# Optimization experiments

Hardware: AMD Instinct MI355X
Metric: run time of the kernel (lower is better)

The kernel has to match this reference:

```python
import jax, jax.numpy as jnp
import numpy as np
from jax import lax

# Module dims (match init_kwargs / input_specs)
CIN, COUT, K, STRIDE = 8, 16, 3, 2
U = V = 32                      # input spatial size (inshape = (CIN, U, V))
UO = VO = U // STRIDE           # 'same' padding with stride -> 16
IN_DIM = CIN * U * V + 1        # 8193 (homogeneous)
OUT_DIM = COUT * UO * VO + 1    # 4097 (homogeneous)
N = 1024                        # batch (columns of x_affine)


def setup_inputs() -> dict:
    key = jax.random.key(0)
    k1, k2, k3, k4, k5 = jax.random.split(key, 5)
    w = jax.random.normal(k1, (COUT, CIN, K, K), dtype=jnp.float32) * 0.1
    b = jax.random.normal(k2, (COUT,), dtype=jnp.float32) * 0.1
    # Keying matrices (dense stand-ins for the sparse keys); scaled to keep values sane.
    A = jax.random.normal(k3, (OUT_DIM, OUT_DIM), dtype=jnp.float32) / np.sqrt(OUT_DIM)
    Ainv = jax.random.normal(k4, (IN_DIM, IN_DIM), dtype=jnp.float32) / np.sqrt(IN_DIM)
    x_affine = jax.random.normal(k5, (IN_DIM, N), dtype=jnp.float32)
    return {"w": w, "b": b, "A": A, "Ainv": Ainv, "x_affine": x_affine}


def _toeplitz_conv_apply(z, w, b):
    """Apply the affine Toeplitz conv matrix T to z of shape (CIN*U*V+1, N).
    T = [[conv, bias], [0, 1]] so T@z = [conv(z[:-1]) + b*z[-1]; z[-1]]."""
    n = z.shape[1]
    hom = z[-1]                                   # (N,) homogeneous row
    x = z[:-1].T.reshape(n, CIN, U, V)            # (N, CIN, U, V)
    y = lax.conv_general_dilated(
        x, w, window_strides=(STRIDE, STRIDE), padding="SAME",
        dimension_numbers=("NCHW", "OIHW", "NCHW"))  # (N, COUT, UO, VO)
    y = y + b[None, :, None, None] * hom[:, None, None, None]
    yf = y.reshape(n, COUT * UO * VO).T           # (COUT*UO*VO, N)
    return jnp.concatenate([yf, hom[None, :]], axis=0)  # (OUT_DIM, N)


def reference(w, b, A, Ainv, x_affine):
    # What @ x = A @ T @ Ainv @ x  (factored; never materializes What)
    z = Ainv @ x_affine                # (IN_DIM, N)
    t = _toeplitz_conv_apply(z, w, b)  # (OUT_DIM, N)
    return A @ t                       # (OUT_DIM, N)
```

## Files before the change

### kernel.cpp

```cpp
#include <hip/hip_runtime.h>

#define IN_DIM 8193
#define OUT_DIM 4097
#define NB 1024
#define M1 8192
#define KP1 8256
#define M2 4096
#define KP2 4160

typedef __attribute__((ext_vector_type(8))) short short8;
typedef __attribute__((ext_vector_type(4))) float f32x4;

__device__ __forceinline__ unsigned short f2bf(float f) {
  unsigned int u = __float_as_uint(f);
  u = (u + 0x7fffu + ((u >> 16) & 1u)) >> 16;
  return (unsigned short)u;
}
__device__ __forceinline__ float bf2f(unsigned short u) {
  return __uint_as_float(((unsigned int)u) << 16);
}

__global__ __launch_bounds__(256) void cvt_pad_kernel(
    const float* __restrict__ src, unsigned short* __restrict__ dst,
    int sR, int sC, int dR, int dC) {
  int gid = blockIdx.x * 256 + threadIdx.x;
  int i4 = gid * 4;
  if (i4 >= dR * dC) return;
  int r = i4 / dC;
  int c = i4 - r * dC;
  unsigned short o[4];
#pragma unroll
  for (int j = 0; j < 4; ++j) {
    int cc = c + j;
    float v = (r < sR && cc < sC) ? src[(size_t)r * sC + cc] : 0.f;
    o[j] = f2bf(v);
  }
  unsigned int lo = (unsigned)o[0] | ((unsigned)o[1] << 16);
  unsigned int hi = (unsigned)o[2] | ((unsigned)o[3] << 16);
  *reinterpret_cast<uint2*>(dst + i4) = make_uint2(lo, hi);
}

__global__ __launch_bounds__(256) void transpose_cvt_zh_kernel(
    const float* __restrict__ src, unsigned short* __restrict__ dst,
    const float* __restrict__ arow, float* __restrict__ zh,
    int K, int N, int Kp) {
  __shared__ float tl[32][33];
  const int ntk = Kp >> 5;
  int bx = blockIdx.x % ntk;
  int by = blockIdx.x / ntk;
  int k0 = bx * 32, n0 = by * 32;
  int tx = threadIdx.x & 31, ty = threadIdx.x >> 5;
#pragma unroll
  for (int i = 0; i < 4; ++i) {
    int k = k0 + ty + i * 8;
    tl[ty + i * 8][tx] = (k < K) ? src[(size_t)k * N + n0 + tx] : 0.f;
  }
  const float av = (k0 + tx < K) ? arow[k0 + tx] : 0.f;
  __syncthreads();
#pragma unroll
  for (int i = 0; i < 4; ++i) {
    int n = n0 + ty + i * 8;
    float v = tl[tx][ty + i * 8];
    dst[(size_t)n * Kp + k0 + tx] = f2bf(v);
    float c = av * v;
#pragma unroll
    for (int m = 1; m <= 16; m <<= 1) c += __shfl_xor(c, m);
    if (tx == 0) atomicAdd(&zh[n], c);
  }
}

__global__ __launch_bounds__(256) void zero_kernel(float4* __restrict__ p, int n) {
  int i = blockIdx.x * 256 + threadIdx.x;
  if (i < n) p[i] = make_float4(0.f, 0.f, 0.f, 0.f);
}

template <int NKT, int NSPLIT, int BMBITS, int MROWS>
__global__ __launch_bounds__(512) void gemm_dp(
    const unsigned short* __restrict__ Ab,
    const unsigned short* __restrict__ Bt,
    float* __restrict__ C, int Kp) {
  extern __shared__ unsigned short lds[];
  const int tid = threadIdx.x;
  const int wid = tid >> 6;
  const int lane = tid & 63;
  const int b = blockIdx.x;
  const int x = b & 7, q = b >> 3;
  const int bm = (q & ((1 << BMBITS) - 1)) * 8 + x;
  const int bn = (q >> BMBITS) & 3;
  const int sp = q >> (BMBITS + 2);
  const int wm = (wid >> 2) << 7;
  const int wn = (wid & 3) << 6;

  const int qk = NKT / NSPLIT, rrk = NKT % NSPLIT;
  const int kt0 = sp * qk + (sp < rrk ? sp : rrk);
  const int T = qk + (sp < rrk ? 1 : 0);
  float* Cp = C + (size_t)sp * MROWS * NB;

  const int g0 = ((lane >> 4) ^ (lane & 7)) * 8;
  const int g1 = ((4 + (lane >> 4)) ^ (lane & 7)) * 8;
  const int alo = (lane & 15) * 64;
  const int bhalf = (wn >> 7) << 1;
  const int ahalf = (wid >> 2) << 1;
  const int bsub = ((wn & 64) << 6) + alo;

#define STAGE(TT, ISA)                                                         \
  do {                                                                         \
    const int tt_ = (TT);                                                      \
    const int kc_ = kt0 + (tt_ < T - 1 ? tt_ : T - 1);                         \
    const int par_ = tt_ & 1;                                                  \
    const unsigned short* M_ = (ISA) ? Ab : Bt;                                \
    const int br_ = ((ISA) ? bm : bn) << 8;                                    \
    _Pragma("unroll")                                                          \
    for (int h_ = 0; h_ < 2; ++h_) {                                           \
      _Pragma("unroll")                                                        \
      for (int L_ = 0; L_ < 2; ++L_) {                                         \
        const int s_ = L_ * 512 + tid;                                         \
        const int row_ = s_ >> 3;                                              \
        const int gl_ = (s_ & 7) ^ (row_ & 7);                                 \
        const unsigned short* g_ = M_ + (size_t)(br_ + (h_ << 7) + row_) * Kp  \
                                      + (kc_ << 6) + gl_ * 8;                  \
        unsigned short* l_ = lds + (((ISA) ? 0 : 4) + (h_ << 1) + par_) * 8192 \
                                 + (size_t)(L_ * 512 + wid * 64) * 8;          \
        __builtin_amdgcn_global_load_lds(                                      \
            (const __attribute__((address_space(1))) void*)g_,                 \
            (__attribute__((address_space(3))) void*)l_, 16, 0, 0);            \
      }                                                                        \
    }                                                                          \
  } while (0)

#define MFMA16(BV0, BV1, NF0, NF1)                                             \
  do {                                                                         \
    __builtin_amdgcn_s_setprio(1);                                             \
    _Pragma("unroll")                                                          \
    for (int mf_ = 0; mf_ < 8; ++mf_) {                                        \
      asm volatile("v_mfma_f32_16x16x32_bf16 %0, %1, %2, %0"                   \
                   : "+v"(acc[mf_][NF0]) : "v"(af[mf_]), "v"(BV0));            \
      asm volatile("v_mfma_f32_16x16x32_bf16 %0, %1, %2, %0"                   \
                   : "+v"(acc[mf_][NF1]) : "v"(af[mf_]), "v"(BV1));            \
    }                                                                          \
    __builtin_amdgcn_s_setprio(0);                                             \
  } while (0)

  f32x4 acc[8][4];
#pragma unroll
  for (int i = 0; i < 8; ++i)
#pragma unroll
    for (int j = 0; j < 4; ++j) acc[i][j] = (f32x4)(0.0f);

  STAGE(0, 1);
  STAGE(0, 0);
  STAGE(1, 1);

  for (int t = 0; t < T; ++t) {
    const int par = t & 1;
    const unsigned short* Ab_ = lds + (ahalf + par) * 8192 + alo;
    const unsigned short* Bb_ = lds + (4 + bhalf + par) * 8192 + bsub;
    short8 af[8], b0, b1;
    __builtin_amdgcn_sched_barrier(0);
    asm volatile("s_waitcnt vmcnt(4)" ::: "memory");
    __builtin_amdgcn_s_barrier();
    __builtin_amdgcn_sched_barrier(0);
    STAGE(t + 1, 0);
#pragma unroll
    for (int mf = 0; mf < 8; ++mf)
      af[mf] = *reinterpret_cast<const short8*>(Ab_ + mf * 1024 + g0);
    b0 = *reinterpret_cast<const short8*>(Bb_ + 0 * 1024 + g0);
    b1 = *reinterpret_cast<const short8*>(Bb_ + 1 * 1024 + g0);
    MFMA16(b0, b1, 0, 1);
    b0 = *reinterpret_cast<const short8*>(Bb_ + 2 * 1024 + g0);
    b1 = *reinterpret_cast<const short8*>(Bb_ + 3 * 1024 + g0);
    MFMA16(b0, b1, 2, 3);
#pragma unroll
    for (int mf = 0; mf < 8; ++mf)
      af[mf] = *reinterpret_cast<const short8*>(Ab_ + mf * 1024 + g1);
    b0 = *reinterpret_cast<const short8*>(Bb_ + 2 * 1024 + g1);
    b1 = *reinterpret_cast<const short8*>(Bb_ + 3 * 1024 + g1);
    MFMA16(b0, b1, 2, 3);
    __builtin_amdgcn_sched_barrier(0);
    __builtin_amdgcn_s_barrier();
    __builtin_amdgcn_sched_barrier(0);
    STAGE(t + 2, 1);
    b0 = *reinterpret_cast<const short8*>(Bb_ + 0 * 1024 + g1);
    b1 = *reinterpret_cast<const short8*>(Bb_ + 1 * 1024 + g1);
    MFMA16(b0, b1, 0, 1);
  }
#undef STAGE
#undef MFMA16

#pragma unroll
  for (int mf = 0; mf < 8; ++mf) {
    const int rb = (bm << 8) + wm + mf * 16 + ((lane >> 4) << 2);
#pragma unroll
    for (int nf = 0; nf < 4; ++nf) {
      const int col = (bn << 8) + wn + nf * 16 + (lane & 15);
#pragma unroll
      for (int r = 0; r < 4; ++r)
        Cp[(size_t)(rb + r) * NB + col] = acc[mf][nf][r];
    }
  }
}

__global__ __launch_bounds__(256) void conv_lds_kernel(
    const float* __restrict__ za, const float* __restrict__ zb,
    const float* __restrict__ zh, const float* __restrict__ w,
    const float* __restrict__ bias, unsigned short* __restrict__ tT) {
  __shared__ float zl[24 * 18 * 32];
  __shared__ float wl[1152];
  __shared__ float bl[16];
  const int b = blockIdx.x;
  const int nt = b & 31, vh = (b >> 5) & 1, uo = b >> 6;
  const int n0 = nt * 32;
  const int tid = threadIdx.x;
#pragma unroll
  for (int it = 0; it < 5; ++it) {
    const int idx = it * 256 + tid;
    if (idx < 1152) wl[idx] = w[idx];
  }
  if (tid < 16) bl[tid] = bias[tid];
  const int nl4 = (tid & 7) * 4;
#pragma unroll
  for (int it = 0; it < 13; ++it) {
    const int R = it * 32 + (tid >> 3);
    if (R < 408) {
      const int ci = R / 51;
      const int rem = R - ci * 51;
      const int kh = rem / 17;
      const int vi = rem - kh * 17;
      const int u = 2 * uo + kh;
      const int v = vh * 16 + vi;
      float4 val = make_float4(0.f, 0.f, 0.f, 0.f);
      if (u < 32 && v < 32) {
        const size_t g = ((size_t)(ci * 1024 + u * 32 + v)) * 1024 + n0 + nl4;
        const float4 a4 = *reinterpret_cast<const float4*>(za + g);
        const float4 b4 = *reinterpret_cast<const float4*>(zb + g);
        val = make_float4(a4.x + b4.x, a4.y + b4.y, a4.z + b4.z, a4.w + b4.w);
      }
      *reinterpret_cast<float4*>(zl + ((ci * 3 + kh) * 18 + vi) * 32 + nl4) = val;
    }
  }
  __syncthreads();
  const int nl = tid & 31;
  const int cop = tid >> 5;
  const float hom = zh[n0 + nl];
  float acc[2][8];
#pragma unroll
  for (int c = 0; c < 2; ++c) {
    const float bb = bl[cop + c * 8] * hom;
#pragma unroll
    for (int vo = 0; vo < 8; ++vo) acc[c][vo] = bb;
  }
  for (int ci = 0; ci < 8; ++ci) {
#pragma unroll
    for (int kh = 0; kh < 3; ++kh) {
      const float* zr = zl + (ci * 3 + kh) * (18 * 32) + nl;
      float zv[17];
#pragma unroll
      for (int vi = 0; vi < 17; ++vi) zv[vi] = zr[vi * 32];
#pragma unroll
      for (int c = 0; c < 2; ++c) {
        const int co = cop + c * 8;
        const float* wp = wl + ((co * 8 + ci) * 3 + kh) * 3;
#pragma unroll
        for (int kw = 0; kw < 3; ++kw) {
          const float wv = wp[kw];
#pragma unroll
          for (int vo = 0; vo < 8; ++vo) acc[c][vo] += wv * zv[2 * vo + kw];
        }
      }
    }
  }
#pragma unroll
  for (int c = 0; c < 2; ++c) {
    const int co = cop + c * 8;
    unsigned short o[8];
#pragma unroll
    for (int vo = 0; vo < 8; ++vo) o[vo] = f2bf(acc[c][vo]);
    uint4 pv;
    pv.x = (unsigned)o[0] | ((unsigned)o[1] << 16);
    pv.y = (unsigned)o[2] | ((unsigned)o[3] << 16);
    pv.z = (unsigned)o[4] | ((unsigned)o[5] << 16);
    pv.w = (unsigned)o[6] | ((unsigned)o[7] << 16);
    *reinterpret_cast<uint4*>(
        tT + (size_t)(n0 + nl) * KP2 + co * 256 + uo * 16 + vh * 8) = pv;
  }
}

__global__ __launch_bounds__(256) void homrow_kernel(
    const float* __restrict__ zh, unsigned short* __restrict__ tT) {
  const int n = blockIdx.x * 256 + threadIdx.x;
  unsigned short* p = tT + (size_t)n * KP2 + 4096;
  uint4 z4 = make_uint4(0u, 0u, 0u, 0u);
  uint4 h4 = z4;
  h4.x = (unsigned)f2bf(zh[n]);
  *reinterpret_cast<uint4*>(p) = h4;
#pragma unroll
  for (int i = 1; i < 8; ++i) *reinterpret_cast<uint4*>(p + i * 8) = z4;
}

__global__ __launch_bounds__(256) void sum4_kernel(
    const float* __restrict__ p, float* __restrict__ out, int n4) {
  const int i = blockIdx.x * 256 + threadIdx.x;
  if (i >= n4) return;
  const size_t stride4 = (size_t)M2 * NB / 4;
  const float4* p4 = (const float4*)p;
  float4 a = p4[i];
  float4 b = p4[i + stride4];
  float4 c = p4[i + 2 * stride4];
  float4 d = p4[i + 3 * stride4];
  float4 r;
  r.x = (a.x + b.x) + (c.x + d.x);
  r.y = (a.y + b.y) + (c.y + d.y);
  r.z = (a.z + b.z) + (c.z + d.z);
  r.w = (a.w + b.w) + (c.w + d.w);
  reinterpret_cast<float4*>(out)[i] = r;
}

__global__ __launch_bounds__(256) void outrow_kernel(
    const unsigned short* __restrict__ A2row,
    const unsigned short* __restrict__ tT, float* __restrict__ out) {
  const int wid = threadIdx.x >> 6, lane = threadIdx.x & 63;
  const int n = blockIdx.x * 4 + wid;
  const unsigned short* trow = tT + (size_t)n * KP2;
  float acc = 0.f;
#pragma unroll
  for (int it = 0; it < 9; ++it) {
    const int i8 = it * 64 + lane;
    if (i8 < KP2 / 8) {
      short8 tv = *reinterpret_cast<const short8*>(trow + i8 * 8);
      short8 av = *reinterpret_cast<const short8*>(A2row + i8 * 8);
#pragma unroll
      for (int j = 0; j < 8; ++j)
        acc += bf2f((unsigned short)tv[j]) * bf2f((unsigned short)av[j]);
    }
  }
#pragma unroll
  for (int m = 1; m <= 32; m <<= 1) acc += __shfl_xor(acc, m);
  if (lane == 0) out[(size_t)4096 * NB + n] = acc;
}

extern "C" void kernel_launch(void* const* d_in, const int* in_sizes, int n_in,
                              void* d_out, int out_size, void* d_ws, size_t ws_size,
                              hipStream_t stream) {
  const float* w    = (const float*)d_in[0];
  const float* bias = (const float*)d_in[1];
  const float* A    = (const float*)d_in[2];
  const float* Ainv = (const float*)d_in[3];
  const float* x    = (const float*)d_in[4];
  float* out = (float*)d_out;

  char* ws = (char*)d_ws;
  const size_t o_xT = (size_t)M1 * KP1 * 2;
  const size_t o_z2 = o_xT + (size_t)NB * KP1 * 2;
  const size_t o_tT = o_z2 + (size_t)2 * M1 * NB * 4;
  const size_t o_zh = o_tT + (size_t)NB * KP2 * 2;
  unsigned short* Ainv_b = (unsigned short*)ws;
  unsigned short* xT_b   = (unsigned short*)(ws + o_xT);
  float*          z2     = (float*)(ws + o_z2);
  unsigned short* tT_b   = (unsigned short*)(ws + o_tT);
  float*          zh     = (float*)(ws + o_zh);
  unsigned short* A2_b   = (unsigned short*)ws;
  float*          outp   = (float*)(ws + (size_t)OUT_DIM * KP2 * 2);
  (void)ws_size; (void)in_sizes; (void)n_in; (void)out_size;

  hipFuncSetAttribute((const void*)gemm_dp<129, 2, 2, M1>,
                      hipFuncAttributeMaxDynamicSharedMemorySize, 131072);
  hipFuncSetAttribute((const void*)gemm_dp<65, 4, 1, M2>,
                      hipFuncAttributeMaxDynamicSharedMemorySize, 131072);

  zero_kernel<<<1, 256, 0, stream>>>((float4*)zh, 256);
  cvt_pad_kernel<<<(M1 * KP1 / 4) / 256, 256, 0, stream>>>(
      Ainv, Ainv_b, IN_DIM, IN_DIM, M1, KP1);
  transpose_cvt_zh_kernel<<<(KP1 / 32) * (NB / 32), 256, 0, stream>>>(
      x, xT_b, Ainv + (size_t)8192 * IN_DIM, zh, IN_DIM, NB, KP1);
  gemm_dp<129, 2, 2, M1><<<256, 512, 131072, stream>>>(
      Ainv_b, xT_b, z2, KP1);
  conv_lds_kernel<<<1024, 256, 0, stream>>>(
      z2, z2 + (size_t)M1 * NB, zh, w, bias, tT_b);
  homrow_kernel<<<4, 256, 0, stream>>>(zh, tT_b);
  cvt_pad_kernel<<<(OUT_DIM * KP2 / 4 + 255) / 256, 256, 0, stream>>>(
      A, A2_b, OUT_DIM, OUT_DIM, OUT_DIM, KP2);
  gemm_dp<65, 4, 1, M2><<<256, 512, 131072, stream>>>(
      A2_b, tT_b, outp, KP2);
  sum4_kernel<<<(M2 * NB / 4) / 256, 256, 0, stream>>>(
      outp, out, M2 * NB / 4);
  outrow_kernel<<<NB / 4, 256, 0, stream>>>(
      A2_b + (size_t)4096 * KP2, tT_b, out);
}
```

Measured before the change: 435.3 us.

## Fuse fp32-to-bf16 conversion of A operands into GEMM register loads

Removes the separate cvt_pad passes that converted Ainv and A into padded bf16 copies in the workspace. The GEMM now loads fp32 A tiles into registers with dword loads, converts them to bf16 and writes them into swizzled LDS, while the B operand keeps its direct global-to-LDS path. This cuts a full read and write of both large matrices plus the extra launches. In exchange the fp32 A data is re-read by each N-block, adds VGPR pressure, and the padded K tail reads past row ends, relying on the zero-padded B to cancel it.

```diff
diff --git a/kernel.cpp b/kernel.cpp
--- a/kernel.cpp
+++ b/kernel.cpp
@@ -18,26 +18,6 @@
 }
 __device__ __forceinline__ float bf2f(unsigned short u) {
   return __uint_as_float(((unsigned int)u) << 16);
-}
-
-__global__ __launch_bounds__(256) void cvt_pad_kernel(
-    const float* __restrict__ src, unsigned short* __restrict__ dst,
-    int sR, int sC, int dR, int dC) {
-  int gid = blockIdx.x * 256 + threadIdx.x;
-  int i4 = gid * 4;
-  if (i4 >= dR * dC) return;
-  int r = i4 / dC;
-  int c = i4 - r * dC;
-  unsigned short o[4];
-#pragma unroll
-  for (int j = 0; j < 4; ++j) {
-    int cc = c + j;
-    float v = (r < sR && cc < sC) ? src[(size_t)r * sC + cc] : 0.f;
-    o[j] = f2bf(v);
-  }
-  unsigned int lo = (unsigned)o[0] | ((unsigned)o[1] << 16);
-  unsigned int hi = (unsigned)o[2] | ((unsigned)o[3] << 16);
-  *reinterpret_cast<uint2*>(dst + i4) = make_uint2(lo, hi);
 }
 
 __global__ __launch_bounds__(256) void transpose_cvt_zh_kernel(
@@ -74,11 +54,24 @@
   if (i < n) p[i] = make_float4(0.f, 0.f, 0.f, 0.f);
 }
 
+#define ALOAD8(R0, R1, R2, R3, R4, R5, R6, R7, P)                             \
+  asm volatile("global_load_dword %0, %8, off\n\t"                            \
+               "global_load_dword %1, %8, off offset:4\n\t"                   \
+               "global_load_dword %2, %8, off offset:8\n\t"                   \
+               "global_load_dword %3, %8, off offset:12\n\t"                  \
+               "global_load_dword %4, %8, off offset:16\n\t"                  \
+               "global_load_dword %5, %8, off offset:20\n\t"                  \
+               "global_load_dword %6, %8, off offset:24\n\t"                  \
+               "global_load_dword %7, %8, off offset:28\n\t"                  \
+               : "=&v"(R0), "=&v"(R1), "=&v"(R2), "=&v"(R3), "=&v"(R4),       \
+                 "=&v"(R5), "=&v"(R6), "=&v"(R7)                              \
+               : "v"(P))
+
 template <int NKT, int NSPLIT, int BMBITS, int MROWS>
-__global__ __launch_bounds__(512) void gemm_dp(
-    const unsigned short* __restrict__ Ab,
+__global__ __launch_bounds__(512) void gemm_fa(
+    const float* __restrict__ Af,
     const unsigned short* __restrict__ Bt,
-    float* __restrict__ C, int Kp) {
+    float* __restrict__ C, int Kact, int Kp) {
   extern __shared__ unsigned short lds[];
   const int tid = threadIdx.x;
   const int wid = tid >> 6;
@@ -103,13 +96,14 @@
   const int ahalf = (wid >> 2) << 1;
   const int bsub = ((wn & 64) << 6) + alo;
 
-#define STAGE(TT, ISA)                                                         \
+  const int arow = tid >> 1;
+  const int acol = (tid & 1) << 5;
+
+#define STAGEB(TT)                                                             \
   do {                                                                         \
     const int tt_ = (TT);                                                      \
     const int kc_ = kt0 + (tt_ < T - 1 ? tt_ : T - 1);                         \
     const int par_ = tt_ & 1;                                                  \
-    const unsigned short* M_ = (ISA) ? Ab : Bt;                                \
-    const int br_ = ((ISA) ? bm : bn) << 8;                                    \
     _Pragma("unroll")                                                          \
     for (int h_ = 0; h_ < 2; ++h_) {                                           \
       _Pragma("unroll")                                                        \
@@ -117,14 +111,45 @@
         const int s_ = L_ * 512 + tid;                                         \
         const int row_ = s_ >> 3;                                              \
         const int gl_ = (s_ & 7) ^ (row_ & 7);                                 \
-        const unsigned short* g_ = M_ + (size_t)(br_ + (h_ << 7) + row_) * Kp  \
-                                      + (kc_ << 6) + gl_ * 8;                  \
-        unsigned short* l_ = lds + (((ISA) ? 0 : 4) + (h_ << 1) + par_) * 8192 \
-                                 + (size_t)(L_ * 512 + wid * 64) * 8;          \
+        const unsigned short* g_ =                                             \
+            Bt + (size_t)((bn << 8) + (h_ << 7) + row_) * Kp + (kc_ << 6) +    \
+            gl_ * 8;                                                           \
+        unsigned short* l_ = lds + (4 + (h_ << 1) + par_) * 8192 +             \
+                             (size_t)(L_ * 512 + wid * 64) * 8;                \
         __builtin_amdgcn_global_load_lds(                                      \
             (const __attribute__((address_space(1))) void*)g_,                 \
             (__attribute__((address_space(3))) void*)l_, 16, 0, 0);            \
       }                                                                        \
+    }                                                                          \
+  } while (0)
+
+#define ALOAD(TT)                                                              \
+  do {                                                                         \
+    const int tt_ = (TT);                                                      \
+    const int kc_ = kt0 + (tt_ < T - 1 ? tt_ : T - 1);                         \
+    const float* p_ =                                                          \
+        Af + (size_t)((bm << 8) + arow) * Kact + (kc_ << 6) + acol;            \
+    ALOAD8(ar[0], ar[1], ar[2], ar[3], ar[4], ar[5], ar[6], ar[7], p_);        \
+    ALOAD8(ar[8], ar[9], ar[10], ar[11], ar[12], ar[13], ar[14], ar[15],       \
+           p_ + 8);                                                            \
+    ALOAD8(ar[16], ar[17], ar[18], ar[19], ar[20], ar[21], ar[22], ar[23],     \
+           p_ + 16);                                                           \
+    ALOAD8(ar[24], ar[25], ar[26], ar[27], ar[28], ar[29], ar[30], ar[31],     \
+           p_ + 24);                                                           \
+  } while (0)
+
+#define ACVT(TT)                                                               \
+  do {                                                                         \
+    const int parw_ = (TT) & 1;                                                \
+    unsigned short* wb_ =                                                      \
+        lds + (((arow >> 7) << 1) + parw_) * 8192 + (arow & 127) * 64;         \
+    _Pragma("unroll")                                                          \
+    for (int j_ = 0; j_ < 4; ++j_) {                                           \
+      short8 pv_;                                                              \
+      _Pragma("unroll")                                                        \
+      for (int c_ = 0; c_ < 8; ++c_) pv_[c_] = (short)f2bf(ar[j_ * 8 + c_]);   \
+      const int ph_ = ((acol >> 3) + j_) ^ (arow & 7);                         \
+      *reinterpret_cast<short8*>(wb_ + ph_ * 8) = pv_;                         \
     }                                                                          \
   } while (0)
 
@@ -147,9 +172,17 @@
 #pragma unroll
     for (int j = 0; j < 4; ++j) acc[i][j] = (f32x4)(0.0f);
 
-  STAGE(0, 1);
-  STAGE(0, 0);
-  STAGE(1, 1);
+  float ar[32];
+  ALOAD(0);
+  __builtin_amdgcn_sched_barrier(0);
+  asm volatile("s_waitcnt vmcnt(0)" ::: "memory");
+  __builtin_amdgcn_sched_barrier(0);
+  ACVT(0);
+  __builtin_amdgcn_sched_barrier(0);
+  STAGEB(0);
+  __builtin_amdgcn_sched_barrier(0);
+  ALOAD(1);
+  __builtin_amdgcn_sched_barrier(0);
 
   for (int t = 0; t < T; ++t) {
     const int par = t & 1;
@@ -157,10 +190,10 @@
     const unsigned short* Bb_ = lds + (4 + bhalf + par) * 8192 + bsub;
     short8 af[8], b0, b1;
     __builtin_amdgcn_sched_barrier(0);
-    asm volatile("s_waitcnt vmcnt(4)" ::: "memory");
+    asm volatile("s_waitcnt vmcnt(32) lgkmcnt(0)" ::: "memory");
     __builtin_amdgcn_s_barrier();
     __builtin_amdgcn_sched_barrier(0);
-    STAGE(t + 1, 0);
+    STAGEB(t + 1);
 #pragma unroll
     for (int mf = 0; mf < 8; ++mf)
       af[mf] = *reinterpret_cast<const short8*>(Ab_ + mf * 1024 + g0);
@@ -179,12 +212,17 @@
     __builtin_amdgcn_sched_barrier(0);
     __builtin_amdgcn_s_barrier();
     __builtin_amdgcn_sched_barrier(0);
-    STAGE(t + 2, 1);
+    asm volatile("s_waitcnt vmcnt(4)" ::: "memory");
+    __builtin_amdgcn_sched_barrier(0);
+    ACVT(t + 1);
+    ALOAD(t + 2);
     b0 = *reinterpret_cast<const short8*>(Bb_ + 0 * 1024 + g1);
     b1 = *reinterpret_cast<const short8*>(Bb_ + 1 * 1024 + g1);
     MFMA16(b0, b1, 0, 1);
   }
-#undef STAGE
+#undef STAGEB
+#undef ALOAD
+#undef ACVT
 #undef MFMA16
 
 #pragma unroll
@@ -316,23 +354,13 @@
 }
 
 __global__ __launch_bounds__(256) void outrow_kernel(
-    const unsigned short* __restrict__ A2row,
-    const unsigned short* __restrict__ tT, float* __restrict__ out) {
+    const float* __restrict__ Arow, const unsigned short* __restrict__ tT,
+    float* __restrict__ out) {
   const int wid = threadIdx.x >> 6, lane = threadIdx.x & 63;
   const int n = blockIdx.x * 4 + wid;
   const unsigned short* trow = tT + (size_t)n * KP2;
   float acc = 0.f;
-#pragma unroll
-  for (int it = 0; it < 9; ++it) {
-    const int i8 = it * 64 + lane;
-    if (i8 < KP2 / 8) {
-      short8 tv = *reinterpret_cast<const short8*>(trow + i8 * 8);
-      short8 av = *reinterpret_cast<const short8*>(A2row + i8 * 8);
-#pragma unroll
-      for (int j = 0; j < 8; ++j)
-        acc += bf2f((unsigned short)tv[j]) * bf2f((unsigned short)av[j]);
-    }
-  }
+  for (int i = lane; i < OUT_DIM; i += 64) acc += Arow[i] * bf2f(trow[i]);
 #pragma unroll
   for (int m = 1; m <= 32; m <<= 1) acc += __shfl_xor(acc, m);
   if (lane == 0) out[(size_t)4096 * NB + n] = acc;
@@ -349,40 +377,34 @@
   float* out = (float*)d_out;
 
   char* ws = (char*)d_ws;
-  const size_t o_xT = (size_t)M1 * KP1 * 2;
-  const size_t o_z2 = o_xT + (size_t)NB * KP1 * 2;
+  const size_t o_z2 = (size_t)NB * KP1 * 2;
   const size_t o_tT = o_z2 + (size_t)2 * M1 * NB * 4;
   const size_t o_zh = o_tT + (size_t)NB * KP2 * 2;
-  unsigned short* Ainv_b = (unsigned short*)ws;
-  unsigned short* xT_b   = (unsigned short*)(ws + o_xT);
-  float*          z2     = (float*)(ws + o_z2);
-  unsigned short* tT_b   = (unsigned short*)(ws + o_tT);
-  float*          zh     = (float*)(ws + o_zh);
-  unsigned short* A2_b   = (unsigned short*)ws;
-  float*          outp   = (float*)(ws + (size_t)OUT_DIM * KP2 * 2);
+  const size_t o_op = o_zh + 4096;
+  unsigned short* xT_b = (unsigned short*)ws;
+  float*          z2   = (float*)(ws + o_z2);
+  unsigned short* tT_b = (unsigned short*)(ws + o_tT);
+  float*          zh   = (float*)(ws + o_zh);
+  float*          outp = (float*)(ws + o_op);
   (void)ws_size; (void)in_sizes; (void)n_in; (void)out_size;
 
-  hipFuncSetAttribute((const void*)gemm_dp<129, 2, 2, M1>,
+  hipFuncSetAttribute((const void*)gemm_fa<129, 2, 2, M1>,
                       hipFuncAttributeMaxDynamicSharedMemorySize, 131072);
-  hipFuncSetAttribute((const void*)gemm_dp<65, 4, 1, M2>,
+  hipFuncSetAttribute((const void*)gemm_fa<65, 4, 1, M2>,
                       hipFuncAttributeMaxDynamicSharedMemorySize, 131072);
 
   zero_kernel<<<1, 256, 0, stream>>>((float4*)zh, 256);
-  cvt_pad_kernel<<<(M1 * KP1 / 4) / 256, 256, 0, stream>>>(
-      Ainv, Ainv_b, IN_DIM, IN_DIM, M1, KP1);
   transpose_cvt_zh_kernel<<<(KP1 / 32) * (NB / 32), 256, 0, stream>>>(
       x, xT_b, Ainv + (size_t)8192 * IN_DIM, zh, IN_DIM, NB, KP1);
-  gemm_dp<129, 2, 2, M1><<<256, 512, 131072, stream>>>(
-      Ainv_b, xT_b, z2, KP1);
+  gemm_fa<129, 2, 2, M1><<<256, 512, 131072, stream>>>(
+      Ainv, xT_b, z2, IN_DIM, KP1);
   conv_lds_kernel<<<1024, 256, 0, stream>>>(
       z2, z2 + (size_t)M1 * NB, zh, w, bias, tT_b);
   homrow_kernel<<<4, 256, 0, stream>>>(zh, tT_b);
-  cvt_pad_kernel<<<(OUT_DIM * KP2 / 4 + 255) / 256, 256, 0, stream>>>(
-      A, A2_b, OUT_DIM, OUT_DIM, OUT_DIM, KP2);
-  gemm_dp<65, 4, 1, M2><<<256, 512, 131072, stream>>>(
-      A2_b, tT_b, outp, KP2);
+  gemm_fa<65, 4, 1, M2><<<256, 512, 131072, stream>>>(
+      A, tT_b, outp, OUT_DIM, KP2);
   sum4_kernel<<<(M2 * NB / 4) / 256, 256, 0, stream>>>(
       outp, out, M2 * NB / 4);
   outrow_kernel<<<NB / 4, 256, 0, stream>>>(
-      A2_b + (size_t)4096 * KP2, tT_b, out);
-}
+      A + (size_t)4096 * OUT_DIM, tT_b, out);
+}
```

New measurement: 681.2 us. +56.5%, slower.

## Split GEMM main loop into four barrier-synced phases interleaving loads with MFMA

Applied to the files above, without the earlier changes.

Restructures the bf16 MFMA GEMM main loop into four phases, each issuing part of the next tile's global-to-LDS loads, then the LDS fragment reads, then a barrier plus lgkmcnt wait before its MFMA block. The B-tile stage is split into two halves spread across phases. The aim is finer-grained interleaving of memory traffic and matrix math across the workgroup, in the style of ping-pong schedules. The cost is many more workgroup barriers per iteration, which can stall waves if the phases are unbalanced.

```diff
diff --git a/kernel.cpp b/kernel.cpp
--- a/kernel.cpp
+++ b/kernel.cpp
@@ -103,7 +103,7 @@
   const int ahalf = (wid >> 2) << 1;
   const int bsub = ((wn & 64) << 6) + alo;
 
-#define STAGE(TT, ISA)                                                         \
+#define STAGEH(TT, ISA, H)                                                     \
   do {                                                                         \
     const int tt_ = (TT);                                                      \
     const int kc_ = kt0 + (tt_ < T - 1 ? tt_ : T - 1);                         \
@@ -111,20 +111,17 @@
     const unsigned short* M_ = (ISA) ? Ab : Bt;                                \
     const int br_ = ((ISA) ? bm : bn) << 8;                                    \
     _Pragma("unroll")                                                          \
-    for (int h_ = 0; h_ < 2; ++h_) {                                           \
-      _Pragma("unroll")                                                        \
-      for (int L_ = 0; L_ < 2; ++L_) {                                         \
-        const int s_ = L_ * 512 + tid;                                         \
-        const int row_ = s_ >> 3;                                              \
-        const int gl_ = (s_ & 7) ^ (row_ & 7);                                 \
-        const unsigned short* g_ = M_ + (size_t)(br_ + (h_ << 7) + row_) * Kp  \
-                                      + (kc_ << 6) + gl_ * 8;                  \
-        unsigned short* l_ = lds + (((ISA) ? 0 : 4) + (h_ << 1) + par_) * 8192 \
-                                 + (size_t)(L_ * 512 + wid * 64) * 8;          \
-        __builtin_amdgcn_global_load_lds(                                      \
-            (const __attribute__((address_space(1))) void*)g_,                 \
-            (__attribute__((address_space(3))) void*)l_, 16, 0, 0);            \
-      }                                                                        \
+    for (int L_ = 0; L_ < 2; ++L_) {                                           \
+      const int s_ = L_ * 512 + tid;                                           \
+      const int row_ = s_ >> 3;                                                \
+      const int gl_ = (s_ & 7) ^ (row_ & 7);                                   \
+      const unsigned short* g_ = M_ + (size_t)(br_ + ((H) << 7) + row_) * Kp   \
+                                    + (kc_ << 6) + gl_ * 8;                    \
+      unsigned short* l_ = lds + (((ISA) ? 0 : 4) + ((H) << 1) + par_) * 8192  \
+                               + (size_t)(L_ * 512 + wid * 64) * 8;            \
+      __builtin_amdgcn_global_load_lds(                                        \
+          (const __attribute__((address_space(1))) void*)g_,                   \
+          (__attribute__((address_space(3))) void*)l_, 16, 0, 0);              \
     }                                                                          \
   } while (0)
 
@@ -141,51 +138,64 @@
     __builtin_amdgcn_s_setprio(0);                                             \
   } while (0)
 
+#define PHASE_SYNC()                                                           \
+  do {                                                                         \
+    __builtin_amdgcn_s_barrier();                                              \
+    asm volatile("s_waitcnt lgkmcnt(0)" ::: "memory");                         \
+    __builtin_amdgcn_sched_barrier(0);                                         \
+  } while (0)
+
   f32x4 acc[8][4];
 #pragma unroll
   for (int i = 0; i < 8; ++i)
 #pragma unroll
     for (int j = 0; j < 4; ++j) acc[i][j] = (f32x4)(0.0f);
 
-  STAGE(0, 1);
-  STAGE(0, 0);
-  STAGE(1, 1);
+  STAGEH(0, 1, 0); STAGEH(0, 1, 1);
+  STAGEH(0, 0, 0); STAGEH(0, 0, 1);
+  STAGEH(1, 1, 0); STAGEH(1, 1, 1);
+  asm volatile("s_waitcnt vmcnt(4)" ::: "memory");
+  __builtin_amdgcn_s_barrier();
 
   for (int t = 0; t < T; ++t) {
     const int par = t & 1;
     const unsigned short* Ab_ = lds + (ahalf + par) * 8192 + alo;
     const unsigned short* Bb_ = lds + (4 + bhalf + par) * 8192 + bsub;
     short8 af[8], b0, b1;
-    __builtin_amdgcn_sched_barrier(0);
-    asm volatile("s_waitcnt vmcnt(4)" ::: "memory");
-    __builtin_amdgcn_s_barrier();
-    __builtin_amdgcn_sched_barrier(0);
-    STAGE(t + 1, 0);
+    STAGEH(t + 1, 0, 0);
 #pragma unroll
     for (int mf = 0; mf < 8; ++mf)
       af[mf] = *reinterpret_cast<const short8*>(Ab_ + mf * 1024 + g0);
     b0 = *reinterpret_cast<const short8*>(Bb_ + 0 * 1024 + g0);
     b1 = *reinterpret_cast<const short8*>(Bb_ + 1 * 1024 + g0);
+    PHASE_SYNC();
     MFMA16(b0, b1, 0, 1);
+    __builtin_amdgcn_s_barrier();
+    STAGEH(t + 1, 0, 1);
     b0 = *reinterpret_cast<const short8*>(Bb_ + 2 * 1024 + g0);
     b1 = *reinterpret_cast<const short8*>(Bb_ + 3 * 1024 + g0);
+    PHASE_SYNC();
     MFMA16(b0, b1, 2, 3);
+    __builtin_amdgcn_s_barrier();
 #pragma unroll
     for (int mf = 0; mf < 8; ++mf)
       af[mf] = *reinterpret_cast<const short8*>(Ab_ + mf * 1024 + g1);
     b0 = *reinterpret_cast<const short8*>(Bb_ + 2 * 1024 + g1);
     b1 = *reinterpret_cast<const short8*>(Bb_ + 3 * 1024 + g1);
+    PHASE_SYNC();
     MFMA16(b0, b1, 2, 3);
-    __builtin_amdgcn_sched_barrier(0);
     __builtin_amdgcn_s_barrier();
-    __builtin_amdgcn_sched_barrier(0);
-    STAGE(t + 2, 1);
+    STAGEH(t + 2, 1, 0); STAGEH(t + 2, 1, 1);
     b0 = *reinterpret_cast<const short8*>(Bb_ + 0 * 1024 + g1);
     b1 = *reinterpret_cast<const short8*>(Bb_ + 1 * 1024 + g1);
+    asm volatile("s_waitcnt vmcnt(4)" ::: "memory");
+    PHASE_SYNC();
     MFMA16(b0, b1, 0, 1);
-  }
-#undef STAGE
+    __builtin_amdgcn_s_barrier();
+  }
+#undef STAGEH
 #undef MFMA16
+#undef PHASE_SYNC
 
 #pragma unroll
   for (int mf = 0; mf < 8; ++mf) {
```

After: 422.4 us (median of 2 runs). 1.03x faster.
